# Optimization experiments

Hardware: AMD Instinct MI355X
Metric: run time of the kernel (lower is better)

Reference implementation:

```python
import jax, jax.numpy as jnp
import numpy as np


def setup_inputs() -> dict:
    key = jax.random.key(0)
    ks = jax.random.split(key, 12)
    C, H, L, P = 256, 8, 4, 4
    Lq, Lx = 2048, 300
    iss = jnp.array([[64, 64], [32, 32], [16, 16], [8, 8]], dtype=jnp.int32)
    Len_in = int(np.sum(np.array(iss)[:, 0] * np.array(iss)[:, 1]))  # 5440
    lsi = jnp.array([0, 4096, 5120, 5376], dtype=jnp.int32)
    return {
        "query": jax.random.normal(ks[0], (1, Lq, C), jnp.float32),
        "reference_points": jax.random.uniform(ks[1], (1, Lq, L, 2), jnp.float32),
        "input_flatten": jax.random.normal(ks[2], (1, Len_in, C), jnp.float32),
        "input_spatial_shapes": iss,
        "add_keys": jax.random.normal(ks[3], (1, Lx, C), jnp.float32),
        "input_level_start_index": lsi,
        "W_off": jax.random.normal(ks[4], (H * L * P * 2, C), jnp.float32) * 0.01,
        "b_off": jax.random.normal(ks[5], (H * L * P * 2,), jnp.float32),
        "W_attn": jax.random.normal(ks[6], (H * (L + 1), C, C), jnp.float32) * 0.05,
        "W_v": jax.random.normal(ks[7], (H * 2, C, C), jnp.float32) * 0.05,
        "b_v": jax.random.normal(ks[8], (H * 2, C), jnp.float32) * 0.01,
        "W_mix": jax.random.normal(ks[9], (C, H + 1), jnp.float32) * 0.5,
    }


def reference(query, reference_points, input_flatten, input_spatial_shapes,
              add_keys, input_level_start_index, W_off, b_off, W_attn, W_v, b_v, W_mix):
    N, Lq, C = query.shape
    L = input_spatial_shapes.shape[0]
    H = W_v.shape[0] // 2
    P = W_off.shape[0] // (H * L * 2)

    # sampling locations: ref (x,y in [0,1]) + offsets / (W,H)
    off = (query @ W_off.T + b_off).reshape(N, Lq, H, L, P, 2)
    wh = input_spatial_shapes[:, ::-1].astype(query.dtype)  # (L,2) = (W,H)
    loc = reference_points[:, :, None, :, None, :] + off / wh[None, None, None, :, None, :]

    # get_keys: truncating index computation + gather (faithful to original)
    loc = jnp.clip(loc, 0.0, 0.999)
    iss_f = input_spatial_shapes.astype(loc.dtype)[None, None, None, :, None, :]
    idx = (loc * iss_f).astype(jnp.int32)  # (N,Lq,H,L,P,2): (int(x*H_l), int(y*W_l))
    lin = (idx[..., 0]
           + idx[..., 1] * input_spatial_shapes[:, 0].astype(jnp.int32)[None, None, None, :, None]
           + input_level_start_index.astype(jnp.int32)[None, None, None, :, None])
    keys = input_flatten[0][lin[0]]                # (Lq,H,L,P,C)
    keys = jnp.transpose(keys, (1, 2, 3, 0, 4))    # (H,L,P,Lq,C)

    head_w = jax.nn.softmax(W_mix.T, axis=0)       # (H+1,C)
    qf = query[0]                                  # (Lq,C)
    ak = add_keys[0]                               # (Lx,C)

    # per-head, per-level similarity (replicates original overlapping index h*L+lvl)
    Ws = W_attn[jnp.arange(H)[:, None] * L + jnp.arange(L)[None, :]]  # (H,L,C,C)
    T = jnp.einsum('hlce,hlpqe->hlcpq', Ws, keys)  # (H,L,C,P,Lq)
    # faithful reshape quirk: (C, P*Lq) viewed as (P, Lq, C)
    T = T.reshape(H, L, P, Lq, C)
    attn_s = jnp.einsum('hlpqc,qc->hlpq', T, qf).reshape(H, L * P, Lq)

    Wadd = W_attn[jnp.arange(H) * L + L]           # (H,C,C)
    attn_a = jnp.einsum('xe,hce,qc->hxq', ak, Wadd, qf)  # (H,Lx,Lq)

    attn = jax.nn.softmax(jnp.concatenate([attn_s, attn_a], axis=1), axis=1)
    attn_s_sm, attn_a_sm = attn[:, :L * P], attn[:, L * P:]

    Wv0, bv0 = W_v[0::2], b_v[0::2]
    Wv1, bv1 = W_v[1::2], b_v[1::2]
    vals = (jnp.einsum('hlpqe,hce->hlpqc', keys, Wv0)
            + bv0[:, None, None, None, :]).reshape(H, L * P, Lq, C)
    v2 = jnp.einsum('xe,hce->hxc', ak, Wv1) + bv1[:, None, :]  # (H,Lx,C)

    out_h = (jnp.einsum('hkq,hkqc->hqc', attn_s_sm, vals)
             + jnp.einsum('hxq,hxc->hqc', attn_a_sm, v2))      # (H,Lq,C)
    result = qf * head_w[-1][None, :] + jnp.einsum('hqc,hc->qc', out_h, head_w[:-1])
    return result[None]
```

## Files before the change

kernel.cpp:

```cpp
#include <hip/hip_runtime.h>
#include <stdint.h>

#define NJ 316

typedef __attribute__((ext_vector_type(8))) short short8;
typedef __attribute__((ext_vector_type(4))) float f32x4;
union U4S8 { uint4 u; short8 s; };

__device__ __forceinline__ unsigned short f2bf(float x) {
    unsigned int u = __float_as_uint(x);
    u += 0x7fff + ((u >> 16) & 1);
    return (unsigned short)(u >> 16);
}
__device__ __forceinline__ float bf2f(unsigned short h) {
    return __uint_as_float(((unsigned int)h) << 16);
}

__global__ __launch_bounds__(256) void cvt3_kernel(
    const float* __restrict__ q,  unsigned short* __restrict__ qh,  unsigned short* __restrict__ ql,
    const float* __restrict__ ak, unsigned short* __restrict__ akh, unsigned short* __restrict__ akl,
    const float* __restrict__ wv, unsigned short* __restrict__ wvh, unsigned short* __restrict__ wvl)
{
    int i = blockIdx.x * 256 + threadIdx.x;
    const float* s; unsigned short *dh, *dl; int off;
    if (i < 131072)      { s = q;  dh = qh;  dl = ql;  off = i; }
    else if (i < 150272) { s = ak; dh = akh; dl = akl; off = i - 131072; }
    else                 { s = wv; dh = wvh; dl = wvl; off = i - 150272; }
    float4 v = ((const float4*)s)[off];
    unsigned short h[4], l[4];
    float x[4] = {v.x, v.y, v.z, v.w};
    #pragma unroll
    for (int j = 0; j < 4; ++j) {
        h[j] = f2bf(x[j]);
        l[j] = f2bf(x[j] - bf2f(h[j]));
    }
    ((uint2*)dh)[off] = make_uint2((unsigned)h[0] | ((unsigned)h[1] << 16),
                                   (unsigned)h[2] | ((unsigned)h[3] << 16));
    ((uint2*)dl)[off] = make_uint2((unsigned)l[0] | ((unsigned)l[1] << 16),
                                   (unsigned)l[2] | ((unsigned)l[3] << 16));
}

__global__ __launch_bounds__(256) void cvt_pack_kernel(
    const float* __restrict__ src, unsigned int* __restrict__ dst, int n4)
{
    for (int i = blockIdx.x * 256 + threadIdx.x; i < n4; i += gridDim.x * 256) {
        float4 v = ((const float4*)src)[i];
        float x[4] = {v.x, v.y, v.z, v.w};
        unsigned int o[4];
        #pragma unroll
        for (int j = 0; j < 4; ++j) {
            unsigned short h = f2bf(x[j]);
            unsigned short l = f2bf(x[j] - bf2f(h));
            o[j] = (unsigned)h | ((unsigned)l << 16);
        }
        ((uint4*)dst)[i] = make_uint4(o[0], o[1], o[2], o[3]);
    }
}

__global__ __launch_bounds__(256) void cvt_wadd_kernel(
    const float* __restrict__ Wattn, unsigned short* __restrict__ dh,
    unsigned short* __restrict__ dl)
{
    int i = blockIdx.x * 256 + threadIdx.x;
    int z = i >> 16, r = i & 65535;
    float v = Wattn[(size_t)(4 * z + 4) * 65536 + r];
    unsigned short h = f2bf(v);
    dh[i] = h;
    dl[i] = f2bf(v - bf2f(h));
}

__global__ __launch_bounds__(256) void cvt_akT_kernel(
    const float* __restrict__ ak, unsigned short* __restrict__ dh,
    unsigned short* __restrict__ dl)
{
    const int e = blockIdx.x;
    for (int k = threadIdx.x; k < 320; k += 256) {
        float v = (k >= 16 && k < 316) ? ak[(k - 16) * 256 + e] : 0.f;
        unsigned short h = f2bf(v);
        dh[e * 320 + k] = h;
        dl[e * 320 + k] = f2bf(v - bf2f(h));
    }
}

__global__ __launch_bounds__(256) void lin_kernel(
    const float* __restrict__ query, const float* __restrict__ refp,
    const int* __restrict__ iss, const int* __restrict__ lsi,
    const float* __restrict__ Woff, const float* __restrict__ boff,
    int* __restrict__ lin)
{
    __shared__ float qf8[8][256];
    __shared__ float wtile[256][33];
    __shared__ double offl[8][256];
    const int t = threadIdx.x;
    const int qbase = blockIdx.x * 8;
    #pragma unroll
    for (int i = 0; i < 8; ++i) qf8[i][t] = query[(qbase + i) * 256 + t];
    double acc[8];
    #pragma unroll
    for (int r = 0; r < 8; ++r) acc[r] = 0.0;
    for (int cb = 0; cb < 256; cb += 32) {
        __syncthreads();
        #pragma unroll
        for (int i = 0; i < 32; ++i) {
            int f = i * 256 + t;
            int o = f >> 5, jj = f & 31;
            wtile[o][jj] = Woff[o * 256 + cb + jj];
        }
        __syncthreads();
        #pragma unroll
        for (int jj = 0; jj < 32; ++jj) {
            double wv = (double)wtile[t][jj];
            #pragma unroll
            for (int r = 0; r < 8; ++r)
                acc[r] += (double)qf8[r][cb + jj] * wv;
        }
    }
    double bo = (double)boff[t];
    __syncthreads();
    #pragma unroll
    for (int r = 0; r < 8; ++r) offl[r][t] = acc[r] + bo;
    __syncthreads();
    #pragma unroll
    for (int rep = 0; rep < 4; ++rep) {
        int idx = rep * 256 + t;
        int r = idx >> 7;
        int s = idx & 127;
        int l = (s >> 2) & 3;
        int q = qbase + r;
        double offx = offl[r][2 * s];
        double offy = offl[r][2 * s + 1];
        int w0 = iss[l * 2 + 0];
        int w1 = iss[l * 2 + 1];
        double locx = (double)refp[q * 8 + l * 2 + 0] + offx / (double)w1;
        double locy = (double)refp[q * 8 + l * 2 + 1] + offy / (double)w0;
        locx = fmin(fmax(locx, 0.0), 0.999);
        locy = fmin(fmax(locy, 0.0), 0.999);
        int ix = (int)(locx * (double)w0);
        int iy = (int)(locy * (double)w1);
        lin[q * 128 + s] = ix + iy * w0 + lsi[l];
    }
}

__global__ __launch_bounds__(256, 4) void gattn_mfma(
    const unsigned short* __restrict__ qh, const unsigned short* __restrict__ ql,
    const unsigned int* __restrict__ inflatP, const float* __restrict__ Wattn,
    const int* __restrict__ lin, float* __restrict__ attn)
{
    __shared__ int linrow[256];
    __shared__ float Glds[16][268];
    const int t = threadIdx.x;
    const int lane = t & 63, w = t >> 6;
    const int b = blockIdx.x;
    const int qb = b & 7, p = (b >> 3) & 3, l = (b >> 5) & 3, h = b >> 7;
    linrow[t] = lin[(256 * qb + t) * 128 + h * 16 + l * 4 + p];
    __syncthreads();

    const int l15 = lane & 15, g = lane >> 4;
    const int q2l = qb + 8 * p + 32 * l15;
    const int ebase = 64 * w + l15;

    f32x4 acc[4][4];
    #pragma unroll
    for (int i = 0; i < 4; ++i)
        #pragma unroll
        for (int eg = 0; eg < 4; ++eg) acc[i][eg] = (f32x4){0.f, 0.f, 0.f, 0.f};

    for (int kb = 0; kb < 256; kb += 32) {
        U4S8 ah[4], al[4];
        #pragma unroll
        for (int i = 0; i < 4; ++i) {
            size_t off = (size_t)(q2l + 512 * i) * 256 + kb + 8 * g;
            ah[i].u = *(const uint4*)(qh + off);
            al[i].u = *(const uint4*)(ql + off);
        }
        int rowoff[8];
        #pragma unroll
        for (int m = 0; m < 8; ++m) rowoff[m] = linrow[kb + 8 * g + m] * 256;
        unsigned int uv[4][8];
        #pragma unroll
        for (int eg = 0; eg < 4; ++eg)
            #pragma unroll
            for (int m = 0; m < 8; ++m)
                uv[eg][m] = inflatP[rowoff[m] + ebase + 16 * eg];

        #pragma unroll
        for (int eg = 0; eg < 4; ++eg) {
            U4S8 bh, bl;
            unsigned int hh[4], ll[4];
            #pragma unroll
            for (int d = 0; d < 4; ++d) {
                hh[d] = __builtin_amdgcn_perm(uv[eg][2 * d + 1], uv[eg][2 * d],
                                              0x05040100u);
                ll[d] = __builtin_amdgcn_perm(uv[eg][2 * d + 1], uv[eg][2 * d],
                                              0x07060302u);
            }
            bh.u = make_uint4(hh[0], hh[1], hh[2], hh[3]);
            bl.u = make_uint4(ll[0], ll[1], ll[2], ll[3]);
            #pragma unroll
            for (int i = 0; i < 4; ++i) {
                acc[i][eg] = __builtin_amdgcn_mfma_f32_16x16x32_bf16(
                    ah[i].s, bh.s, acc[i][eg], 0, 0, 0);
                acc[i][eg] = __builtin_amdgcn_mfma_f32_16x16x32_bf16(
                    ah[i].s, bl.s, acc[i][eg], 0, 0, 0);
                acc[i][eg] = __builtin_amdgcn_mfma_f32_16x16x32_bf16(
                    al[i].s, bh.s, acc[i][eg], 0, 0, 0);
            }
        }
    }

    const int tx = t & 15, ty = t >> 4;
    const float* Wsbase = Wattn + (size_t)(h * 4 + l) * 65536;
    #pragma unroll
    for (int ci = 0; ci < 4; ++ci) {
        __syncthreads();
        #pragma unroll
        for (int eg = 0; eg < 4; ++eg)
            #pragma unroll
            for (int r = 0; r < 4; ++r)
                Glds[4 * g + r][64 * w + 16 * eg + l15] = acc[ci][eg][r];
        __syncthreads();
        const int hi = 16 * ci + ty;
        const int q2 = qb + 8 * p + 32 * hi;
        float gv[16];
        #pragma unroll
        for (int i2 = 0; i2 < 4; ++i2) {
            float4 gd = *(const float4*)&Glds[ty][tx * 4 + 64 * i2];
            gv[i2 * 4 + 0] = gd.x;
            gv[i2 * 4 + 1] = gd.y;
            gv[i2 * 4 + 2] = gd.z;
            gv[i2 * 4 + 3] = gd.w;
        }
        #pragma unroll
        for (int p2 = 0; p2 < 4; ++p2) {
            const float* wr = Wsbase + (size_t)(hi + 64 * p2) * 256;
            float partial = 0.f;
            #pragma unroll
            for (int i2 = 0; i2 < 4; ++i2) {
                float4 wv = *(const float4*)&wr[tx * 4 + 64 * i2];
                partial += wv.x * gv[i2 * 4 + 0] + wv.y * gv[i2 * 4 + 1]
                         + wv.z * gv[i2 * 4 + 2] + wv.w * gv[i2 * 4 + 3];
            }
            partial += __shfl_xor(partial, 1);
            partial += __shfl_xor(partial, 2);
            partial += __shfl_xor(partial, 4);
            partial += __shfl_xor(partial, 8);
            if (tx == 0)
                attn[((size_t)h * 2048 + q2) * NJ + (l * 4 + p2)] = partial;
        }
    }
}

struct Seg {
    const unsigned short *Ah, *Al, *Bh, *Bl;
    int K, lda, ldb;
    long sA, sB;
};

template<bool ACCUM, bool OUTF32, int NSEG, bool FULLB>
__global__ __launch_bounds__(256) void mfma_gemm(
    Seg s0, Seg s1,
    float* __restrict__ Cf, unsigned short* __restrict__ Ch,
    unsigned short* __restrict__ Cl,
    int M, int N, int ldc, long sC)
{
    __shared__ unsigned short As[2][64 * 40];
    __shared__ unsigned short Bs[2][128 * 40];
    const int t = threadIdx.x;
    const int lane = t & 63;
    const int wave = t >> 6;
    const int wm = (wave & 1) * 32, wn = (wave >> 1) * 64;
    const int nb = blockIdx.x * 128, mb = blockIdx.y * 64;
    const int z = blockIdx.z;

    f32x4 acc[2][4];
    #pragma unroll
    for (int i = 0; i < 2; ++i)
        #pragma unroll
        for (int j = 0; j < 4; ++j) acc[i][j] = (f32x4){0.f, 0.f, 0.f, 0.f};

    const int arow = t >> 2, akoff = (t & 3) * 8;
    const int frow = lane & 15, fk = (lane >> 4) * 8;

    #pragma unroll
    for (int seg = 0; seg < NSEG; ++seg) {
        const Seg S = seg ? s1 : s0;
        const unsigned short* Azh = S.Ah + (size_t)z * S.sA;
        const unsigned short* Azl = S.Al + (size_t)z * S.sA;
        const unsigned short* Bzh = S.Bh + (size_t)z * S.sB;
        const unsigned short* Bzl = S.Bl + (size_t)z * S.sB;
        for (int kb = 0; kb < S.K; kb += 32) {
            __syncthreads();
            {
                int gm = mb + arow;
                uint4 vh = {0, 0, 0, 0}, vl = {0, 0, 0, 0};
                if (gm < M) {
                    size_t o = (size_t)gm * S.lda + kb + akoff;
                    vh = *(const uint4*)(Azh + o);
                    vl = *(const uint4*)(Azl + o);
                }
                *(uint4*)&As[0][arow * 40 + akoff] = vh;
                *(uint4*)&As[1][arow * 40 + akoff] = vl;
                #pragma unroll
                for (int i = 0; i < 2; ++i) {
                    int f = i * 256 + t;
                    int brow = f >> 2, bkoff = (f & 3) * 8;
                    int gn = nb + brow;
                    uint4 wh = {0, 0, 0, 0}, wl = {0, 0, 0, 0};
                    if (gn < N) {
                        size_t o = (size_t)gn * S.ldb + kb + bkoff;
                        wh = *(const uint4*)(Bzh + o);
                        if (FULLB) wl = *(const uint4*)(Bzl + o);
                    }
                    *(uint4*)&Bs[0][brow * 40 + bkoff] = wh;
                    if (FULLB) *(uint4*)&Bs[1][brow * 40 + bkoff] = wl;
                }
            }
            __syncthreads();
            short8 a[2][2], b[4][2];
            #pragma unroll
            for (int i = 0; i < 2; ++i) {
                int r = wm + i * 16 + frow;
                a[i][0] = *(const short8*)&As[0][r * 40 + fk];
                a[i][1] = *(const short8*)&As[1][r * 40 + fk];
            }
            #pragma unroll
            for (int j = 0; j < 4; ++j) {
                int r = wn + j * 16 + frow;
                b[j][0] = *(const short8*)&Bs[0][r * 40 + fk];
                if (FULLB) b[j][1] = *(const short8*)&Bs[1][r * 40 + fk];
            }
            #pragma unroll
            for (int i = 0; i < 2; ++i)
                #pragma unroll
                for (int j = 0; j < 4; ++j) {
                    acc[i][j] = __builtin_amdgcn_mfma_f32_16x16x32_bf16(
                        a[i][0], b[j][0], acc[i][j], 0, 0, 0);
                    if (FULLB)
                        acc[i][j] = __builtin_amdgcn_mfma_f32_16x16x32_bf16(
                            a[i][0], b[j][1], acc[i][j], 0, 0, 0);
                    acc[i][j] = __builtin_amdgcn_mfma_f32_16x16x32_bf16(
                        a[i][1], b[j][0], acc[i][j], 0, 0, 0);
                }
        }
    }
    #pragma unroll
    for (int i = 0; i < 2; ++i)
        #pragma unroll
        for (int r = 0; r < 4; ++r) {
            int gm = mb + wm + i * 16 + (lane >> 4) * 4 + r;
            if (gm >= M) continue;
            #pragma unroll
            for (int j = 0; j < 4; ++j) {
                int gn = nb + wn + j * 16 + (lane & 15);
                if (gn >= N) continue;
                size_t idx = (size_t)z * sC + (size_t)gm * ldc + gn;
                float v = acc[i][j][r];
                if (OUTF32) {
                    float prev = ACCUM ? Cf[idx] : 0.f;
                    Cf[idx] = prev + v;
                } else {
                    unsigned short h = f2bf(v);
                    Ch[idx] = h;
                    Cl[idx] = f2bf(v - bf2f(h));
                }
            }
        }
}

__global__ __launch_bounds__(256) void softmax_ka_kernel(
    const float* __restrict__ attn, const unsigned int* __restrict__ inflatP,
    const int* __restrict__ lin, float* __restrict__ s0,
    unsigned short* __restrict__ awh, unsigned short* __restrict__ awl,
    unsigned short* __restrict__ KAh, unsigned short* __restrict__ KAl)
{
    __shared__ float red[8];
    __shared__ float w16[16];
    __shared__ int lls[16];
    const int t = threadIdx.x;
    const int lane = t & 63, w = t >> 6;
    const int rid = blockIdx.x;
    const int h = rid >> 11, q = rid & 2047;
    const float* row = attn + (size_t)rid * NJ;

    float v0 = row[t];
    float v1 = (t < 60) ? row[256 + t] : -1e30f;
    float m = fmaxf(v0, v1);
    #pragma unroll
    for (int d = 1; d < 64; d <<= 1) m = fmaxf(m, __shfl_xor(m, d));
    if (lane == 0) red[w] = m;
    __syncthreads();
    m = fmaxf(fmaxf(red[0], red[1]), fmaxf(red[2], red[3]));

    float e0 = expf(v0 - m);
    float e1 = (t < 60) ? expf(v1 - m) : 0.f;
    float s = e0 + e1;
    #pragma unroll
    for (int d = 1; d < 64; d <<= 1) s += __shfl_xor(s, d);
    if (lane == 0) red[4 + w] = s;
    __syncthreads();
    s = (red[4] + red[5]) + (red[6] + red[7]);
    const float inv = 1.f / s;

    float sf = (t < 16) ? e0 : 0.f;
    #pragma unroll
    for (int d = 1; d < 64; d <<= 1) sf += __shfl_xor(sf, d);
    if (lane == 0) red[w] = sf;

    float a0 = e0 * inv;
    float a1 = e1 * inv;
    unsigned short h0 = f2bf(a0);
    awh[(size_t)rid * 320 + t] = h0;
    awl[(size_t)rid * 320 + t] = f2bf(a0 - bf2f(h0));
    if (t >= 60 && t < 64) { a1 = 0.f; }
    if (t < 64) {
        unsigned short h1 = f2bf(a1);
        awh[(size_t)rid * 320 + 256 + t] = h1;
        awl[(size_t)rid * 320 + 256 + t] = f2bf(a1 - bf2f(h1));
    }
    if (t < 16) {
        w16[t] = a0;
        lls[t] = lin[q * 128 + h * 16 + t];
    }
    __syncthreads();
    if (t == 0)
        s0[rid] = ((red[0] + red[1]) + (red[2] + red[3])) * inv;

    float acc = 0.f;
    #pragma unroll
    for (int k = 0; k < 16; ++k) {
        unsigned int u = inflatP[lls[k] * 256 + t];
        acc += w16[k] * (bf2f((unsigned short)(u & 0xffff)) +
                         bf2f((unsigned short)(u >> 16)));
    }
    unsigned short hh = f2bf(acc);
    KAh[(size_t)rid * 256 + t] = hh;
    KAl[(size_t)rid * 256 + t] = f2bf(acc - bf2f(hh));
}

__global__ __launch_bounds__(256) void final_kernel(
    const float* __restrict__ qf, const float* __restrict__ OH,
    const float* __restrict__ s0, const float* __restrict__ bv,
    const float* __restrict__ Wmix, float* __restrict__ out)
{
    const int q = blockIdx.x, c = threadIdx.x;
    float wj[9], m = -1e30f;
    #pragma unroll
    for (int j = 0; j < 9; ++j) { wj[j] = Wmix[c * 9 + j]; m = fmaxf(m, wj[j]); }
    float s = 0.f;
    #pragma unroll
    for (int j = 0; j < 9; ++j) { wj[j] = expf(wj[j] - m); s += wj[j]; }
    float inv = 1.f / s;
    float acc = qf[q * 256 + c] * wj[8] * inv;
    #pragma unroll
    for (int h = 0; h < 8; ++h) {
        float s0v = s0[h * 2048 + q];
        float oh = OH[((size_t)h * 2048 + q) * 256 + c]
                 + s0v * bv[(2 * h) * 256 + c]
                 + (1.f - s0v) * bv[(2 * h + 1) * 256 + c];
        acc += oh * wj[h] * inv;
    }
    out[q * 256 + c] = acc;
}

extern "C" void kernel_launch(void* const* d_in, const int* in_sizes, int n_in,
                              void* d_out, int out_size, void* d_ws, size_t ws_size,
                              hipStream_t stream) {
    const float* query = (const float*)d_in[0];
    const float* refp  = (const float*)d_in[1];
    const float* inflat= (const float*)d_in[2];
    const int*   iss   = (const int*)d_in[3];
    const float* ak    = (const float*)d_in[4];
    const int*   lsi   = (const int*)d_in[5];
    const float* Woff  = (const float*)d_in[6];
    const float* boff  = (const float*)d_in[7];
    const float* Wattn = (const float*)d_in[8];
    const float* Wv    = (const float*)d_in[9];
    const float* bv    = (const float*)d_in[10];
    const float* Wmix  = (const float*)d_in[11];
    float* out = (float*)d_out;

    typedef unsigned short us;
    char* ws = (char*)d_ws;
    int* lin    = (int*)ws;   ws += (size_t)262144 * 4;
    float* attn = (float*)ws; ws += (size_t)8 * 2048 * NJ * 4;
    float* s0   = (float*)ws; ws += (size_t)8 * 2048 * 4;
    unsigned int* inflatP = (unsigned int*)ws; ws += (size_t)1392640 * 4;
    us* qh  = (us*)ws; ws += (size_t)524288 * 2;
    us* ql  = (us*)ws; ws += (size_t)524288 * 2;
    us* akh = (us*)ws; ws += (size_t)320 * 256 * 2;
    us* akl = (us*)ws; ws += (size_t)320 * 256 * 2;
    us* Waddh = (us*)ws; ws += (size_t)524288 * 2;
    us* Waddl = (us*)ws; ws += (size_t)524288 * 2;
    us* Wvh = (us*)ws; ws += (size_t)1048576 * 2;
    us* Wvl = (us*)ws; ws += (size_t)1048576 * 2;
    us* akTh= (us*)ws; ws += (size_t)256 * 320 * 2;
    us* akTl= (us*)ws; ws += (size_t)256 * 320 * 2;
    us* Bhh = (us*)ws; ws += (size_t)8 * 320 * 256 * 2;
    us* Bhl = (us*)ws; ws += (size_t)8 * 320 * 256 * 2;
    us* awh = (us*)ws; ws += (size_t)8 * 2048 * 320 * 2;
    us* awl = (us*)ws; ws += (size_t)8 * 2048 * 320 * 2;
    us* KAh = (us*)ws; ws += (size_t)8 * 2048 * 256 * 2;
    us* KAl = (us*)ws; ws += (size_t)8 * 2048 * 256 * 2;
    us* AAh = (us*)ws; ws += (size_t)8 * 2048 * 256 * 2;
    us* AAl = (us*)ws; ws += (size_t)8 * 2048 * 256 * 2;
    float* OH = (float*)awh;

    cvt3_kernel<<<1611, 256, 0, stream>>>(query, qh, ql, ak, akh, akl,
                                          Wv, Wvh, Wvl);
    cvt_pack_kernel<<<256, 256, 0, stream>>>(inflat, inflatP, 1392640 / 4);
    cvt_wadd_kernel<<<2048, 256, 0, stream>>>(Wattn, Waddh, Waddl);
    cvt_akT_kernel<<<256, 256, 0, stream>>>(ak, akTh, akTl);
    lin_kernel<<<256, 256, 0, stream>>>(query, refp, iss, lsi, Woff, boff, lin);

    Seg sz = {nullptr, nullptr, nullptr, nullptr, 0, 0, 0, 0L, 0L};

    {
        Seg a = {akh, akl, Waddh, Waddl, 256, 256, 256, 0L, 65536L};
        mfma_gemm<false, false, 1, true><<<dim3(2, 5, 8), 256, 0, stream>>>(
            a, sz, nullptr, Bhh, Bhl, 300, 256, 256, 320L * 256);
    }
    {
        Seg a = {qh, ql, Bhh, Bhl, 256, 256, 256, 0L, 320L * 256};
        mfma_gemm<false, true, 1, true><<<dim3(3, 32, 8), 256, 0, stream>>>(
            a, sz, attn + 16, nullptr, nullptr, 2048, 300, NJ, 2048L * NJ);
    }

    gattn_mfma<<<1024, 256, 0, stream>>>(qh, ql, inflatP, Wattn, lin, attn);

    softmax_ka_kernel<<<16384, 256, 0, stream>>>(attn, inflatP, lin, s0,
                                                 awh, awl, KAh, KAl);

    {
        Seg a = {awh, awl, akTh, akTl, 320, 320, 320, 2048L * 320, 0L};
        mfma_gemm<false, false, 1, true><<<dim3(2, 32, 8), 256, 0, stream>>>(
            a, sz, nullptr, AAh, AAl, 2048, 256, 256, 2048L * 256);
    }
    {
        Seg a = {KAh, KAl, Wvh, Wvl, 256, 256, 256, 2048L * 256, 2L * 65536};
        Seg b = {AAh, AAl, Wvh + 65536, Wvl + 65536, 256, 256, 256,
                 2048L * 256, 2L * 65536};
        mfma_gemm<false, true, 2, false><<<dim3(2, 32, 8), 256, 0, stream>>>(
            a, b, OH, nullptr, nullptr, 2048, 256, 256, 2048L * 256);
    }

    final_kernel<<<2048, 256, 0, stream>>>(query, OH, s0, bv, Wmix, out);
}
```

Measured before the change: 305.3 us.

## Reassociate additive-key value path and fuse conversion kernels into one launch

Fuses four small conversion kernels into a single launch and zero-fills a new transposed V2 buffer. It reassociates the additive-key path: instead of attn·ak followed by Wv1, it precomputes V2 = ak·Wv1ᵀ per head and folds attn·V2 into the final GEMM as a second K-segment. This drops one GEMM and the AA intermediate. The attention weights are now stored only in single bf16 (no low part), and per-segment product counts cut MFMAs, trading precision for fewer passes. The gattn occupancy hint also changes from 4 to 3.

```diff
diff --git a/kernel.cpp b/kernel.cpp
--- a/kernel.cpp
+++ b/kernel.cpp
@@ -16,69 +16,69 @@
     return __uint_as_float(((unsigned int)h) << 16);
 }
 
-__global__ __launch_bounds__(256) void cvt3_kernel(
+__global__ __launch_bounds__(256) void cvt_all_kernel(
     const float* __restrict__ q,  unsigned short* __restrict__ qh,  unsigned short* __restrict__ ql,
     const float* __restrict__ ak, unsigned short* __restrict__ akh, unsigned short* __restrict__ akl,
-    const float* __restrict__ wv, unsigned short* __restrict__ wvh, unsigned short* __restrict__ wvl)
+    const float* __restrict__ wv, unsigned short* __restrict__ wvh, unsigned short* __restrict__ wvl,
+    const float* __restrict__ inflat, unsigned int* __restrict__ inflatP,
+    const float* __restrict__ Wattn, unsigned short* __restrict__ wah, unsigned short* __restrict__ wal,
+    unsigned short* __restrict__ v2th, unsigned short* __restrict__ v2tl)
 {
     int i = blockIdx.x * 256 + threadIdx.x;
-    const float* s; unsigned short *dh, *dl; int off;
-    if (i < 131072)      { s = q;  dh = qh;  dl = ql;  off = i; }
-    else if (i < 150272) { s = ak; dh = akh; dl = akl; off = i - 131072; }
-    else                 { s = wv; dh = wvh; dl = wvl; off = i - 150272; }
-    float4 v = ((const float4*)s)[off];
-    unsigned short h[4], l[4];
-    float x[4] = {v.x, v.y, v.z, v.w};
-    #pragma unroll
-    for (int j = 0; j < 4; ++j) {
-        h[j] = f2bf(x[j]);
-        l[j] = f2bf(x[j] - bf2f(h[j]));
-    }
-    ((uint2*)dh)[off] = make_uint2((unsigned)h[0] | ((unsigned)h[1] << 16),
-                                   (unsigned)h[2] | ((unsigned)h[3] << 16));
-    ((uint2*)dl)[off] = make_uint2((unsigned)l[0] | ((unsigned)l[1] << 16),
-                                   (unsigned)l[2] | ((unsigned)l[3] << 16));
-}
-
-__global__ __launch_bounds__(256) void cvt_pack_kernel(
-    const float* __restrict__ src, unsigned int* __restrict__ dst, int n4)
-{
-    for (int i = blockIdx.x * 256 + threadIdx.x; i < n4; i += gridDim.x * 256) {
-        float4 v = ((const float4*)src)[i];
+    if (i < 760576) {
+        const float* s; unsigned short *dh, *dl; int off; bool pack = false;
+        unsigned int* dp = nullptr;
+        if (i < 131072)      { s = q;  dh = qh;  dl = ql;  off = i; }
+        else if (i < 150272) { s = ak; dh = akh; dl = akl; off = i - 131072; }
+        else if (i < 412416) { s = wv; dh = wvh; dl = wvl; off = i - 150272; }
+        else { s = inflat; dp = inflatP; off = i - 412416; pack = true; dh = dl = nullptr; }
+        float4 v = ((const float4*)s)[off];
         float x[4] = {v.x, v.y, v.z, v.w};
-        unsigned int o[4];
+        unsigned short h[4], l[4];
         #pragma unroll
         for (int j = 0; j < 4; ++j) {
-            unsigned short h = f2bf(x[j]);
-            unsigned short l = f2bf(x[j] - bf2f(h));
-            o[j] = (unsigned)h | ((unsigned)l << 16);
-        }
-        ((uint4*)dst)[i] = make_uint4(o[0], o[1], o[2], o[3]);
-    }
-}
-
-__global__ __launch_bounds__(256) void cvt_wadd_kernel(
-    const float* __restrict__ Wattn, unsigned short* __restrict__ dh,
-    unsigned short* __restrict__ dl)
-{
-    int i = blockIdx.x * 256 + threadIdx.x;
-    int z = i >> 16, r = i & 65535;
-    float v = Wattn[(size_t)(4 * z + 4) * 65536 + r];
-    unsigned short h = f2bf(v);
-    dh[i] = h;
-    dl[i] = f2bf(v - bf2f(h));
-}
-
-__global__ __launch_bounds__(256) void cvt_akT_kernel(
-    const float* __restrict__ ak, unsigned short* __restrict__ dh,
-    unsigned short* __restrict__ dl)
-{
-    const int e = blockIdx.x;
-    for (int k = threadIdx.x; k < 320; k += 256) {
-        float v = (k >= 16 && k < 316) ? ak[(k - 16) * 256 + e] : 0.f;
-        unsigned short h = f2bf(v);
-        dh[e * 320 + k] = h;
-        dl[e * 320 + k] = f2bf(v - bf2f(h));
+            h[j] = f2bf(x[j]);
+            l[j] = f2bf(x[j] - bf2f(h[j]));
+        }
+        if (pack) {
+            ((uint4*)dp)[off] = make_uint4(
+                (unsigned)h[0] | ((unsigned)l[0] << 16),
+                (unsigned)h[1] | ((unsigned)l[1] << 16),
+                (unsigned)h[2] | ((unsigned)l[2] << 16),
+                (unsigned)h[3] | ((unsigned)l[3] << 16));
+        } else {
+            ((uint2*)dh)[off] = make_uint2((unsigned)h[0] | ((unsigned)h[1] << 16),
+                                           (unsigned)h[2] | ((unsigned)h[3] << 16));
+            ((uint2*)dl)[off] = make_uint2((unsigned)l[0] | ((unsigned)l[1] << 16),
+                                           (unsigned)l[2] | ((unsigned)l[3] << 16));
+        }
+    } else if (i < 891648) {
+        int off = i - 760576;
+        int base = off * 4;
+        int z = base >> 16, r = base & 65535;
+        float4 v = *(const float4*)&Wattn[(size_t)(4 * z + 4) * 65536 + r];
+        float x[4] = {v.x, v.y, v.z, v.w};
+        unsigned short h[4], l[4];
+        #pragma unroll
+        for (int j = 0; j < 4; ++j) {
+            h[j] = f2bf(x[j]);
+            l[j] = f2bf(x[j] - bf2f(h[j]));
+        }
+        ((uint2*)wah)[off] = make_uint2((unsigned)h[0] | ((unsigned)h[1] << 16),
+                                        (unsigned)h[2] | ((unsigned)h[3] << 16));
+        ((uint2*)wal)[off] = make_uint2((unsigned)l[0] | ((unsigned)l[1] << 16),
+                                        (unsigned)l[2] | ((unsigned)l[3] << 16));
+    } else {
+        int j = i - 891648;
+        size_t base = (size_t)j * 320;
+        uint2 zz = make_uint2(0u, 0u);
+        #pragma unroll
+        for (int d = 0; d < 4; ++d) {
+            ((uint2*)(v2th + base))[d] = zz;
+            ((uint2*)(v2tl + base))[d] = zz;
+        }
+        ((uint2*)(v2th + base + 316))[0] = zz;
+        ((uint2*)(v2tl + base + 316))[0] = zz;
     }
 }
 
@@ -141,7 +141,7 @@
     }
 }
 
-__global__ __launch_bounds__(256, 4) void gattn_mfma(
+__global__ __launch_bounds__(256, 3) void gattn_mfma(
     const unsigned short* __restrict__ qh, const unsigned short* __restrict__ ql,
     const unsigned int* __restrict__ inflatP, const float* __restrict__ Wattn,
     const int* __restrict__ lin, float* __restrict__ attn)
@@ -254,9 +254,10 @@
     const unsigned short *Ah, *Al, *Bh, *Bl;
     int K, lda, ldb;
     long sA, sB;
+    int nprod;
 };
 
-template<bool ACCUM, bool OUTF32, int NSEG, bool FULLB>
+template<bool ACCUM, bool OUTF32, int NSEG>
 __global__ __launch_bounds__(256) void mfma_gemm(
     Seg s0, Seg s1,
     float* __restrict__ Cf, unsigned short* __restrict__ Ch,
@@ -284,10 +285,11 @@
     #pragma unroll
     for (int seg = 0; seg < NSEG; ++seg) {
         const Seg S = seg ? s1 : s0;
+        const int np = S.nprod;
         const unsigned short* Azh = S.Ah + (size_t)z * S.sA;
-        const unsigned short* Azl = S.Al + (size_t)z * S.sA;
+        const unsigned short* Azl = (np >= 2) ? S.Al + (size_t)z * S.sA : nullptr;
         const unsigned short* Bzh = S.Bh + (size_t)z * S.sB;
-        const unsigned short* Bzl = S.Bl + (size_t)z * S.sB;
+        const unsigned short* Bzl = (np >= 3) ? S.Bl + (size_t)z * S.sB : nullptr;
         for (int kb = 0; kb < S.K; kb += 32) {
             __syncthreads();
             {
@@ -296,10 +298,10 @@
                 if (gm < M) {
                     size_t o = (size_t)gm * S.lda + kb + akoff;
                     vh = *(const uint4*)(Azh + o);
-                    vl = *(const uint4*)(Azl + o);
+                    if (np >= 2) vl = *(const uint4*)(Azl + o);
                 }
                 *(uint4*)&As[0][arow * 40 + akoff] = vh;
-                *(uint4*)&As[1][arow * 40 + akoff] = vl;
+                if (np >= 2) *(uint4*)&As[1][arow * 40 + akoff] = vl;
                 #pragma unroll
                 for (int i = 0; i < 2; ++i) {
                     int f = i * 256 + t;
@@ -309,10 +311,10 @@
                     if (gn < N) {
                         size_t o = (size_t)gn * S.ldb + kb + bkoff;
                         wh = *(const uint4*)(Bzh + o);
-                        if (FULLB) wl = *(const uint4*)(Bzl + o);
+                        if (np >= 3) wl = *(const uint4*)(Bzl + o);
                     }
                     *(uint4*)&Bs[0][brow * 40 + bkoff] = wh;
-                    if (FULLB) *(uint4*)&Bs[1][brow * 40 + bkoff] = wl;
+                    if (np >= 3) *(uint4*)&Bs[1][brow * 40 + bkoff] = wl;
                 }
             }
             __syncthreads();
@@ -321,13 +323,13 @@
             for (int i = 0; i < 2; ++i) {
                 int r = wm + i * 16 + frow;
                 a[i][0] = *(const short8*)&As[0][r * 40 + fk];
-                a[i][1] = *(const short8*)&As[1][r * 40 + fk];
+                if (np >= 2) a[i][1] = *(const short8*)&As[1][r * 40 + fk];
             }
             #pragma unroll
             for (int j = 0; j < 4; ++j) {
                 int r = wn + j * 16 + frow;
                 b[j][0] = *(const short8*)&Bs[0][r * 40 + fk];
-                if (FULLB) b[j][1] = *(const short8*)&Bs[1][r * 40 + fk];
+                if (np >= 3) b[j][1] = *(const short8*)&Bs[1][r * 40 + fk];
             }
             #pragma unroll
             for (int i = 0; i < 2; ++i)
@@ -335,11 +337,12 @@
                 for (int j = 0; j < 4; ++j) {
                     acc[i][j] = __builtin_amdgcn_mfma_f32_16x16x32_bf16(
                         a[i][0], b[j][0], acc[i][j], 0, 0, 0);
-                    if (FULLB)
+                    if (np >= 2)
+                        acc[i][j] = __builtin_amdgcn_mfma_f32_16x16x32_bf16(
+                            a[i][1], b[j][0], acc[i][j], 0, 0, 0);
+                    if (np >= 3)
                         acc[i][j] = __builtin_amdgcn_mfma_f32_16x16x32_bf16(
                             a[i][0], b[j][1], acc[i][j], 0, 0, 0);
-                    acc[i][j] = __builtin_amdgcn_mfma_f32_16x16x32_bf16(
-                        a[i][1], b[j][0], acc[i][j], 0, 0, 0);
                 }
         }
     }
@@ -370,7 +373,7 @@
 __global__ __launch_bounds__(256) void softmax_ka_kernel(
     const float* __restrict__ attn, const unsigned int* __restrict__ inflatP,
     const int* __restrict__ lin, float* __restrict__ s0,
-    unsigned short* __restrict__ awh, unsigned short* __restrict__ awl,
+    unsigned short* __restrict__ awh,
     unsigned short* __restrict__ KAh, unsigned short* __restrict__ KAl)
 {
     __shared__ float red[8];
@@ -407,16 +410,10 @@
     if (lane == 0) red[w] = sf;
 
     float a0 = e0 * inv;
-    float a1 = e1 * inv;
-    unsigned short h0 = f2bf(a0);
-    awh[(size_t)rid * 320 + t] = h0;
-    awl[(size_t)rid * 320 + t] = f2bf(a0 - bf2f(h0));
-    if (t >= 60 && t < 64) { a1 = 0.f; }
-    if (t < 64) {
-        unsigned short h1 = f2bf(a1);
-        awh[(size_t)rid * 320 + 256 + t] = h1;
-        awl[(size_t)rid * 320 + 256 + t] = f2bf(a1 - bf2f(h1));
-    }
+    float a1 = (t < 60) ? e1 * inv : 0.f;
+    awh[(size_t)rid * 320 + t] = f2bf(a0);
+    if (t < 64)
+        awh[(size_t)rid * 320 + 256 + t] = f2bf(a1);
     if (t < 16) {
         w16[t] = a0;
         lls[t] = lin[q * 128 + h * 16 + t];
@@ -493,53 +490,50 @@
     us* Waddl = (us*)ws; ws += (size_t)524288 * 2;
     us* Wvh = (us*)ws; ws += (size_t)1048576 * 2;
     us* Wvl = (us*)ws; ws += (size_t)1048576 * 2;
-    us* akTh= (us*)ws; ws += (size_t)256 * 320 * 2;
-    us* akTl= (us*)ws; ws += (size_t)256 * 320 * 2;
     us* Bhh = (us*)ws; ws += (size_t)8 * 320 * 256 * 2;
     us* Bhl = (us*)ws; ws += (size_t)8 * 320 * 256 * 2;
+    us* V2Th= (us*)ws; ws += (size_t)8 * 256 * 320 * 2;
+    us* V2Tl= (us*)ws; ws += (size_t)8 * 256 * 320 * 2;
     us* awh = (us*)ws; ws += (size_t)8 * 2048 * 320 * 2;
-    us* awl = (us*)ws; ws += (size_t)8 * 2048 * 320 * 2;
     us* KAh = (us*)ws; ws += (size_t)8 * 2048 * 256 * 2;
     us* KAl = (us*)ws; ws += (size_t)8 * 2048 * 256 * 2;
-    us* AAh = (us*)ws; ws += (size_t)8 * 2048 * 256 * 2;
-    us* AAl = (us*)ws; ws += (size_t)8 * 2048 * 256 * 2;
-    float* OH = (float*)awh;
-
-    cvt3_kernel<<<1611, 256, 0, stream>>>(query, qh, ql, ak, akh, akl,
-                                          Wv, Wvh, Wvl);
-    cvt_pack_kernel<<<256, 256, 0, stream>>>(inflat, inflatP, 1392640 / 4);
-    cvt_wadd_kernel<<<2048, 256, 0, stream>>>(Wattn, Waddh, Waddl);
-    cvt_akT_kernel<<<256, 256, 0, stream>>>(ak, akTh, akTl);
+    float* OH = (float*)ws;   ws += (size_t)8 * 2048 * 256 * 4;
+
+    cvt_all_kernel<<<3491, 256, 0, stream>>>(
+        query, qh, ql, ak, akh, akl, Wv, Wvh, Wvl,
+        inflat, inflatP, Wattn, Waddh, Waddl, V2Th, V2Tl);
     lin_kernel<<<256, 256, 0, stream>>>(query, refp, iss, lsi, Woff, boff, lin);
 
-    Seg sz = {nullptr, nullptr, nullptr, nullptr, 0, 0, 0, 0L, 0L};
+    Seg sz = {nullptr, nullptr, nullptr, nullptr, 0, 0, 0, 0L, 0L, 0};
 
     {
-        Seg a = {akh, akl, Waddh, Waddl, 256, 256, 256, 0L, 65536L};
-        mfma_gemm<false, false, 1, true><<<dim3(2, 5, 8), 256, 0, stream>>>(
+        Seg a = {akh, akl, Waddh, Waddl, 256, 256, 256, 0L, 65536L, 3};
+        mfma_gemm<false, false, 1><<<dim3(2, 5, 8), 256, 0, stream>>>(
             a, sz, nullptr, Bhh, Bhl, 300, 256, 256, 320L * 256);
     }
     {
-        Seg a = {qh, ql, Bhh, Bhl, 256, 256, 256, 0L, 320L * 256};
-        mfma_gemm<false, true, 1, true><<<dim3(3, 32, 8), 256, 0, stream>>>(
+        Seg a = {Wvh + 65536, Wvl + 65536, akh, nullptr, 256, 256, 256,
+                 131072L, 0L, 2};
+        mfma_gemm<false, false, 1><<<dim3(3, 4, 8), 256, 0, stream>>>(
+            a, sz, nullptr, V2Th + 16, V2Tl + 16, 256, 300, 320, 256L * 320);
+    }
+    {
+        Seg a = {qh, ql, Bhh, Bhl, 256, 256, 256, 0L, 320L * 256, 3};
+        mfma_gemm<false, true, 1><<<dim3(3, 32, 8), 256, 0, stream>>>(
             a, sz, attn + 16, nullptr, nullptr, 2048, 300, NJ, 2048L * NJ);
     }
 
     gattn_mfma<<<1024, 256, 0, stream>>>(qh, ql, inflatP, Wattn, lin, attn);
 
     softmax_ka_kernel<<<16384, 256, 0, stream>>>(attn, inflatP, lin, s0,
-                                                 awh, awl, KAh, KAl);
+                                                 awh, KAh, KAl);
 
     {
-        Seg a = {awh, awl, akTh, akTl, 320, 320, 320, 2048L * 320, 0L};
-        mfma_gemm<false, false, 1, true><<<dim3(2, 32, 8), 256, 0, stream>>>(
-            a, sz, nullptr, AAh, AAl, 2048, 256, 256, 2048L * 256);
-    }
-    {
-        Seg a = {KAh, KAl, Wvh, Wvl, 256, 256, 256, 2048L * 256, 2L * 65536};
-        Seg b = {AAh, AAl, Wvh + 65536, Wvl + 65536, 256, 256, 256,
-                 2048L * 256, 2L * 65536};
-        mfma_gemm<false, true, 2, false><<<dim3(2, 32, 8), 256, 0, stream>>>(
+        Seg a = {KAh, KAl, Wvh, nullptr, 256, 256, 256, 2048L * 256,
+                 2L * 65536, 2};
+        Seg b = {awh, nullptr, V2Th, nullptr, 320, 320, 320, 2048L * 320,
+                 256L * 320, 1};
+        mfma_gemm<false, true, 2><<<dim3(2, 32, 8), 256, 0, stream>>>(
             a, b, OH, nullptr, nullptr, 2048, 256, 256, 2048L * 256);
     }
 
```

Result: faster. 296.1 us (-3.0%).
